# Performance work log

Hardware: AMD Instinct MI355X
Metric: run time of the kernel (lower is better)

Reference implementation:

```python
import jax, jax.numpy as jnp
import numpy as np

NUM_HEADS = 8  # matches init_kwargs


def setup_inputs() -> dict:
    key = jax.random.key(0)
    k_x, k_q, k_k, k_v, k_o = jax.random.split(key, 5)
    C = 512
    scale = 1.0 / np.sqrt(C).astype(np.float32)
    return {
        "x": jax.random.normal(k_x, (4, C, 1024), dtype=jnp.float32),
        "Wq": jax.random.normal(k_q, (C, C), dtype=jnp.float32) * scale,
        "Wk": jax.random.normal(k_k, (C, C), dtype=jnp.float32) * scale,
        "Wv": jax.random.normal(k_v, (C, C), dtype=jnp.float32) * scale,
        "Wo": jax.random.normal(k_o, (C, C), dtype=jnp.float32) * scale,
    }


def reference(x, Wq, Wk, Wv, Wo):
    # x: (b, C, n). Conv1d with kernel size 1 and no bias == channel matmul.
    b, C, n = x.shape
    H = NUM_HEADS
    d = C // H  # truncated_planes

    # 1x1 conv projections: (o, c) x (b, c, n) -> (b, o, n)
    q = jnp.einsum("oc,bcn->bon", Wq, x).reshape(b * H, d, n)
    k = jnp.einsum("oc,bcn->bon", Wk, x).reshape(b * H, d, n)
    v = jnp.einsum("oc,bcn->bon", Wv, x).reshape(b * H, d, n)

    # SelfAttention, embedded-gaussian mode (non-local block style, no 1/sqrt(d) scale):
    # scores[bh, i, j] = q[:, i] . k[:, j]; softmax over j; y = attn @ v
    scores = jnp.einsum("hdi,hdj->hij", q, k)       # (b*H, n, n)
    attn = jax.nn.softmax(scores, axis=-1)
    y = jnp.einsum("hij,hdj->hdi", attn, v)          # (b*H, d, n)

    y = y.reshape(b, C, n)
    out = jnp.einsum("oc,bcn->bon", Wo, y)           # final 1x1 conv
    return out
```

## Files before the change

### kernel.cpp

```cpp
#include <hip/hip_runtime.h>
#include <hip/hip_bf16.h>

typedef __attribute__((ext_vector_type(8))) short short8;
typedef __attribute__((ext_vector_type(8))) _Float16 half8;
typedef __attribute__((ext_vector_type(4))) float floatx4;

#define MFMA_BF16(a,b,c) __builtin_amdgcn_mfma_f32_16x16x32_bf16((a),(b),(c),0,0,0)
#define MFMA_F16(a,b,c)  __builtin_amdgcn_mfma_f32_16x16x32_f16((a),(b),(c),0,0,0)

__device__ __forceinline__ unsigned short f2bf(float f) {
    union { float f; unsigned u; } v; v.f = f;
    unsigned r = (v.u + 0x7fffu + ((v.u >> 16) & 1u)) >> 16;
    return (unsigned short)r;
}
__device__ __forceinline__ float bf2f(unsigned short h) {
    union { unsigned u; float f; } v; v.u = ((unsigned)h) << 16;
    return v.f;
}
__device__ __forceinline__ unsigned short f2h(float f) {
    union { _Float16 h; unsigned short u; } v; v.h = (_Float16)f;
    return v.u;
}
__device__ __forceinline__ float h2f(unsigned short u) {
    union { unsigned short u; _Float16 h; } v; v.u = u;
    return (float)v.h;
}

__device__ __forceinline__ void gll16(const unsigned short* g, unsigned short* l) {
    __builtin_amdgcn_global_load_lds(
        (const __attribute__((address_space(1))) void*)g,
        (__attribute__((address_space(3))) void*)l, 16, 0, 0);
}

__global__ __launch_bounds__(256) void prep_kernel(
    const void* __restrict__ x,
    const void* __restrict__ Wq, const void* __restrict__ Wk,
    const void* __restrict__ Wv, const void* __restrict__ Wo,
    unsigned short* __restrict__ xTh, unsigned short* __restrict__ xTl,
    unsigned short* __restrict__ Wqh, unsigned short* __restrict__ Wkh,
    unsigned short* __restrict__ Wvh, unsigned short* __restrict__ Woh,
    int* __restrict__ flag)
{
    __shared__ float tile[64][65];
    __shared__ int sflag;
    const int tid = threadIdx.x;

    if (tid < 64) {
        unsigned short u = ((const unsigned short*)x)[2 * tid];
        int e = (u >> 7) & 0xFF;
        bool plaus = (e >= 96 && e <= 140);
        unsigned long long m = __ballot(plaus);
        if (tid == 0) sflag = (__popcll(m) >= 40) ? 0 : 1;
    }
    __syncthreads();
    const int isf32 = sflag;
    const int bid = blockIdx.x;
    if (bid == 0 && tid == 0) *flag = isf32;

    if (bid < 512) {
        const int b  = bid >> 7;
        const int rem = bid & 127;
        const int c0 = (rem >> 4) * 64;
        const int n0 = (rem & 15) * 64;
        const int r = tid >> 6, col = tid & 63;
        const size_t base = (size_t)b * 512 * 1024;
        #pragma unroll
        for (int i = 0; i < 16; ++i) {
            int c = i * 4 + r;
            size_t idx = base + (size_t)(c0 + c) * 1024 + n0 + col;
            float v = isf32 ? ((const float*)x)[idx] : bf2f(((const unsigned short*)x)[idx]);
            tile[c][col] = v;
        }
        __syncthreads();
        #pragma unroll
        for (int i = 0; i < 16; ++i) {
            int n = i * 4 + r;
            float v = tile[col][n];
            unsigned short hi = f2h(v);
            size_t idx = ((size_t)b * 1024 + n0 + n) * 512 + c0 + col;
            xTh[idx] = hi;
            xTl[idx] = f2h(v - h2f(hi));
        }
    } else {
        const int b2 = bid - 512;
        #pragma unroll
        for (int m = 0; m < 4; ++m) {
            const void* src = (m == 0) ? Wq : (m == 1) ? Wk : (m == 2) ? Wv : Wo;
            unsigned short* dh = (m == 0) ? Wqh : (m == 1) ? Wkh : (m == 2) ? Wvh : Woh;
            #pragma unroll
            for (int j = 0; j < 16; ++j) {
                int i = b2 * 4096 + j * 256 + tid;
                float v = isf32 ? ((const float*)src)[i] : bf2f(((const unsigned short*)src)[i]);
                dh[i] = f2h(v);
            }
        }
    }
}

__device__ __forceinline__ void stage_qk(
    const unsigned short* __restrict__ Ah, const unsigned short* __restrict__ Al,
    const unsigned short* __restrict__ B,
    unsigned short* L, int k0, int wave, int srow, int koff)
{
    #pragma unroll
    for (int i = 0; i < 4; ++i) {
        int idx = wave + i * 4;
        const unsigned short* s;
        if (idx < 4)      s = Ah + (idx * 16 + srow) * 512 + k0 + koff;
        else if (idx < 8) s = Al + ((idx - 4) * 16 + srow) * 512 + k0 + koff;
        else              s = B + ((idx - 8) * 16 + srow) * 512 + k0 + koff;
        gll16(s, L + idx * 512);
    }
}

__device__ __forceinline__ void gemm_qk(
    const unsigned short* __restrict__ Ah, const unsigned short* __restrict__ Al,
    const unsigned short* __restrict__ B,
    unsigned short* lds, floatx4 acc[2][4], int lane, int wave)
{
    const int quad = lane >> 4, l16 = lane & 15;
    const int msub = (wave & 1) * 32, nsub = (wave >> 1) * 64;
    const int srow = lane >> 2;
    const int koff = (((lane & 3) - (srow >> 1)) & 3) * 8;
    const int pA = ((quad + (l16 >> 1)) & 3) * 8;

    stage_qk(Ah, Al, B, lds, 0, wave, srow, koff);
    for (int k0 = 0; k0 < 512; k0 += 32) {
        __syncthreads();
        unsigned short* L = lds + ((k0 >> 5) & 1) * 8192;
        if (k0 + 32 < 512)
            stage_qk(Ah, Al, B, lds + (((k0 >> 5) + 1) & 1) * 8192,
                     k0 + 32, wave, srow, koff);

        half8 ah[2], al[2], bh[4];
        #pragma unroll
        for (int mt = 0; mt < 2; ++mt) {
            int off = (msub + mt * 16 + l16) * 32 + pA;
            ah[mt] = *(const half8*)(L + off);
            al[mt] = *(const half8*)(L + 2048 + off);
        }
        #pragma unroll
        for (int nt = 0; nt < 4; ++nt)
            bh[nt] = *(const half8*)(L + 4096 + (nsub + nt * 16 + l16) * 32 + pA);
        #pragma unroll
        for (int mt = 0; mt < 2; ++mt)
            #pragma unroll
            for (int nt = 0; nt < 4; ++nt) {
                acc[mt][nt] = MFMA_F16(ah[mt], bh[nt], acc[mt][nt]);
                acc[mt][nt] = MFMA_F16(al[mt], bh[nt], acc[mt][nt]);
            }
    }
}

__device__ __forceinline__ void stage_1t(
    const unsigned short* __restrict__ A, const unsigned short* __restrict__ B,
    unsigned short* L, int k0, int wave, int srow, int koff)
{
    #pragma unroll
    for (int i = 0; i < 3; ++i) {
        int idx = wave + i * 4;
        const unsigned short* s;
        if (idx < 4) s = A + (idx * 16 + srow) * 512 + k0 + koff;
        else         s = B + ((idx - 4) * 16 + srow) * 512 + k0 + koff;
        gll16(s, L + idx * 512);
    }
}

__device__ __forceinline__ void gemm_1t(
    const unsigned short* __restrict__ A, const unsigned short* __restrict__ B,
    unsigned short* lds, floatx4 acc[2][4], int lane, int wave)
{
    const int quad = lane >> 4, l16 = lane & 15;
    const int msub = (wave & 1) * 32, nsub = (wave >> 1) * 64;
    const int srow = lane >> 2;
    const int koff = (((lane & 3) - (srow >> 1)) & 3) * 8;
    const int pA = ((quad + (l16 >> 1)) & 3) * 8;

    stage_1t(A, B, lds, 0, wave, srow, koff);
    for (int k0 = 0; k0 < 512; k0 += 32) {
        __syncthreads();
        unsigned short* L = lds + ((k0 >> 5) & 1) * 6144;
        if (k0 + 32 < 512)
            stage_1t(A, B, lds + (((k0 >> 5) + 1) & 1) * 6144,
                     k0 + 32, wave, srow, koff);

        half8 ah[2], bh[4];
        #pragma unroll
        for (int mt = 0; mt < 2; ++mt)
            ah[mt] = *(const half8*)(L + (msub + mt * 16 + l16) * 32 + pA);
        #pragma unroll
        for (int nt = 0; nt < 4; ++nt)
            bh[nt] = *(const half8*)(L + 2048 + (nsub + nt * 16 + l16) * 32 + pA);
        #pragma unroll
        for (int mt = 0; mt < 2; ++mt)
            #pragma unroll
            for (int nt = 0; nt < 4; ++nt)
                acc[mt][nt] = MFMA_F16(ah[mt], bh[nt], acc[mt][nt]);
    }
}

__global__ __launch_bounds__(256) void proj_kernel(
    const unsigned short* __restrict__ xTh, const unsigned short* __restrict__ xTl,
    const unsigned short* __restrict__ Wqh, const unsigned short* __restrict__ Wkh,
    const unsigned short* __restrict__ Wvh,
    unsigned short* __restrict__ qT, unsigned short* __restrict__ kT,
    unsigned short* __restrict__ vbuf)
{
    __shared__ unsigned short lds[16384];
    const int lane = threadIdx.x & 63;
    const int wave = threadIdx.x >> 6;
    const int quad = lane >> 4, l16 = lane & 15;
    const int idx = blockIdx.x;
    const int msub = (wave & 1) * 32, nsub = (wave >> 1) * 64;

    floatx4 acc[2][4];
    #pragma unroll
    for (int i = 0; i < 2; ++i)
        #pragma unroll
        for (int j = 0; j < 4; ++j) acc[i][j] = (floatx4){0.f, 0.f, 0.f, 0.f};

    if (idx < 512) {
        const int w = idx >> 8;
        const int rem = idx & 255;
        const int m0 = (rem >> 2) * 64;
        const int oblk = (rem & 3) * 128;
        gemm_qk(xTh + (size_t)m0 * 512, xTl + (size_t)m0 * 512,
                ((w == 0) ? Wqh : Wkh) + oblk * 512, lds, acc, lane, wave);

        unsigned short* dst = (w == 0) ? qT : kT;
        #pragma unroll
        for (int mt = 0; mt < 2; ++mt)
            #pragma unroll
            for (int r = 0; r < 4; ++r) {
                int row = m0 + msub + mt * 16 + quad * 4 + r;
                int b = row >> 10, n = row & 1023;
                #pragma unroll
                for (int nt = 0; nt < 4; ++nt) {
                    int o = oblk + nsub + nt * 16 + l16;
                    int head = b * 8 + (o >> 6);
                    int dd = o & 63;
                    dst[(head * 1024 + n) * 64 + dd] = f2h(acc[mt][nt][r]);
                }
            }
    } else {
        const int rem = idx - 512;
        const int m0 = (rem >> 5) * 64;
        const int nblk = (rem & 31) * 128;
        gemm_1t(Wvh + m0 * 512, xTh + (size_t)nblk * 512, lds, acc, lane, wave);

        #pragma unroll
        for (int mt = 0; mt < 2; ++mt)
            #pragma unroll
            for (int r = 0; r < 4; ++r) {
                int o = m0 + msub + mt * 16 + quad * 4 + r;
                #pragma unroll
                for (int nt = 0; nt < 4; ++nt) {
                    int col = nblk + nsub + nt * 16 + l16;
                    int b = col >> 10, n = col & 1023;
                    vbuf[b * (512 * 1024) + o * 1024 + n] = f2bf(acc[mt][nt][r]);
                }
            }
    }
}

__global__ __launch_bounds__(256) void attn_kernel(
    const unsigned short* __restrict__ qT, const unsigned short* __restrict__ kT,
    const unsigned short* __restrict__ vbuf,
    unsigned short* __restrict__ yT)
{
    __shared__ unsigned short lds[20992];
    const int lane = threadIdx.x & 63;
    const int wave = threadIdx.x >> 6;
    const int quad = lane >> 4, l16 = lane & 15;
    const int head = blockIdx.x;
    const int i0 = blockIdx.y * 64 + wave * 16;
    const int b = head >> 3, h = head & 7;
    const unsigned short* qp = qT + head * (1024 * 64);
    const unsigned short* kp = kT + head * (1024 * 64);
    const unsigned short* vb = vbuf + b * (512 * 1024) + h * (64 * 1024);
    const int srow = lane >> 2;
    const int koff = (((lane & 3) - (srow >> 1)) & 3) * 8;
    const int pA = ((quad + (l16 >> 1)) & 3) * 8;

    const int qoff = (i0 + l16) * 64 + quad * 8;
    half8 aq0 = *(const half8*)(qp + qoff);
    half8 aq1 = *(const half8*)(qp + qoff + 32);

    float lacc[4];
    floatx4 oacc[4];
    #pragma unroll
    for (int r = 0; r < 4; ++r) lacc[r] = 0.f;
    #pragma unroll
    for (int dt = 0; dt < 4; ++dt) oacc[dt] = (floatx4){0.f, 0.f, 0.f, 0.f};

    unsigned short* myp = lds + 16384 + wave * 1152;
    const float L2E = 1.44269504f;
    const float C2  = 69.2493619f;

    auto stage_kv = [&](int j0, unsigned short* L) {
        #pragma unroll
        for (int i = 0; i < 4; ++i) {
            int c = wave + i * 4;
            const unsigned short* s;
            if (c < 8) {
                int kc = c >> 2, r0 = (c & 3) * 16;
                s = kp + (j0 + r0 + srow) * 64 + kc * 32 + koff;
            } else {
                int c8 = c - 8; int js = c8 >> 2, r0 = (c8 & 3) * 16;
                s = vb + (r0 + srow) * 1024 + j0 + js * 32 + koff;
            }
            gll16(s, L + c * 512);
        }
    };

    stage_kv(0, lds);

    for (int j0 = 0; j0 < 1024; j0 += 64) {
        __syncthreads();
        unsigned short* L = lds + ((j0 >> 6) & 1) * 8192;
        if (j0 + 64 < 1024)
            stage_kv(j0 + 64, lds + (((j0 >> 6) + 1) & 1) * 8192);

        floatx4 sc[4];
        #pragma unroll
        for (int jt = 0; jt < 4; ++jt) {
            int off = jt * 512 + l16 * 32 + pA;
            half8 kh0 = *(const half8*)(L + off);
            half8 kh1 = *(const half8*)(L + 2048 + off);
            floatx4 s = {0.f, 0.f, 0.f, 0.f};
            s = MFMA_F16(aq0, kh0, s);
            s = MFMA_F16(aq1, kh1, s);
            sc[jt] = s;
        }

        #pragma unroll
        for (int jt = 0; jt < 4; ++jt)
            #pragma unroll
            for (int r = 0; r < 4; ++r) {
                float p = __builtin_amdgcn_exp2f(sc[jt][r] * L2E - C2);
                lacc[r] += p;
                myp[(quad * 4 + r) * 72 + jt * 16 + l16] = f2bf(p);
            }
        __asm__ volatile("s_waitcnt lgkmcnt(0)" ::: "memory");
        short8 pa0 = *(const short8*)(myp + l16 * 72 + quad * 8);
        short8 pa1 = *(const short8*)(myp + l16 * 72 + 32 + quad * 8);

        #pragma unroll
        for (int dt = 0; dt < 4; ++dt) {
            int off = dt * 512 + l16 * 32 + pA;
            short8 bv0 = *(const short8*)(L + 4096 + off);
            short8 bv1 = *(const short8*)(L + 4096 + 2048 + off);
            oacc[dt] = MFMA_BF16(pa0, bv0, oacc[dt]);
            oacc[dt] = MFMA_BF16(pa1, bv1, oacc[dt]);
        }
    }

    float linv[4];
    #pragma unroll
    for (int r = 0; r < 4; ++r) {
        float l = lacc[r];
        l += __shfl_xor(l, 1);
        l += __shfl_xor(l, 2);
        l += __shfl_xor(l, 4);
        l += __shfl_xor(l, 8);
        linv[r] = 1.0f / l;
    }
    #pragma unroll
    for (int dt = 0; dt < 4; ++dt)
        #pragma unroll
        for (int r = 0; r < 4; ++r) {
            int c = h * 64 + dt * 16 + l16;
            int n = i0 + quad * 4 + r;
            yT[((size_t)b * 1024 + n) * 512 + c] = f2h(oacc[dt][r] * linv[r]);
        }
}

__global__ __launch_bounds__(256) void out_kernel(
    const unsigned short* __restrict__ Woh, const unsigned short* __restrict__ yT,
    void* __restrict__ out, const int* __restrict__ flag)
{
    __shared__ unsigned short lds[8192];
    const int isf32 = *flag;
    const int lane = threadIdx.x & 63;
    const int wave = threadIdx.x >> 6;
    const int quad = lane >> 4, l16 = lane & 15;
    const int nblk = blockIdx.x * 64;
    const int oblk = blockIdx.y * 64;
    const unsigned short* A = Woh + oblk * 512;
    const unsigned short* B = yT + (size_t)nblk * 512;
    const int msub = (wave & 1) * 32, nsub = (wave >> 1) * 32;
    const int srow = lane >> 2;
    const int koff = (((lane & 3) - (srow >> 1)) & 3) * 8;
    const int pA = ((quad + (l16 >> 1)) & 3) * 8;

    floatx4 acc[2][2];
    #pragma unroll
    for (int i = 0; i < 2; ++i)
        #pragma unroll
        for (int j = 0; j < 2; ++j) acc[i][j] = (floatx4){0.f, 0.f, 0.f, 0.f};

    auto stage = [&](int k0, unsigned short* L) {
        #pragma unroll
        for (int i = 0; i < 2; ++i) {
            int idx = wave + i * 4;
            const unsigned short* s = (idx < 4)
                ? A + (idx * 16 + srow) * 512 + k0 + koff
                : B + ((idx - 4) * 16 + srow) * 512 + k0 + koff;
            gll16(s, L + idx * 512);
        }
    };

    stage(0, lds);
    for (int k0 = 0; k0 < 512; k0 += 32) {
        __syncthreads();
        unsigned short* L = lds + ((k0 >> 5) & 1) * 4096;
        if (k0 + 32 < 512)
            stage(k0 + 32, lds + (((k0 >> 5) + 1) & 1) * 4096);

        half8 ah[2], bh[2];
        #pragma unroll
        for (int mt = 0; mt < 2; ++mt)
            ah[mt] = *(const half8*)(L + (msub + mt * 16 + l16) * 32 + pA);
        #pragma unroll
        for (int nt = 0; nt < 2; ++nt)
            bh[nt] = *(const half8*)(L + 2048 + (nsub + nt * 16 + l16) * 32 + pA);
        #pragma unroll
        for (int mt = 0; mt < 2; ++mt)
            #pragma unroll
            for (int nt = 0; nt < 2; ++nt)
                acc[mt][nt] = MFMA_F16(ah[mt], bh[nt], acc[mt][nt]);
    }

    #pragma unroll
    for (int mt = 0; mt < 2; ++mt)
        #pragma unroll
        for (int r = 0; r < 4; ++r) {
            int o = oblk + msub + mt * 16 + quad * 4 + r;
            #pragma unroll
            for (int nt = 0; nt < 2; ++nt) {
                int col = nblk + nsub + nt * 16 + l16;
                int b = col >> 10, n = col & 1023;
                size_t di = (size_t)b * (512 * 1024) + o * 1024 + n;
                if (isf32) ((float*)out)[di] = acc[mt][nt][r];
                else       ((unsigned short*)out)[di] = f2bf(acc[mt][nt][r]);
            }
        }
}

extern "C" void kernel_launch(void* const* d_in, const int* in_sizes, int n_in,
                              void* d_out, int out_size, void* d_ws, size_t ws_size,
                              hipStream_t stream)
{
    const void* x  = d_in[0];
    const void* Wq = d_in[1];
    const void* Wk = d_in[2];
    const void* Wv = d_in[3];
    const void* Wo = d_in[4];

    const int NX = 4 * 512 * 1024;
    const int NW = 512 * 512;

    char* p = (char*)d_ws;
    int* flag = (int*)p; p += 64;
    unsigned short* xTh = (unsigned short*)p; p += (size_t)NX * 2;
    unsigned short* xTl = (unsigned short*)p; p += (size_t)NX * 2;
    unsigned short* Wqh = (unsigned short*)p; p += (size_t)NW * 2;
    unsigned short* Wkh = (unsigned short*)p; p += (size_t)NW * 2;
    unsigned short* Wvh = (unsigned short*)p; p += (size_t)NW * 2;
    unsigned short* Woh = (unsigned short*)p; p += (size_t)NW * 2;
    unsigned short* qT  = (unsigned short*)p; p += (size_t)NX * 2;
    unsigned short* kT  = (unsigned short*)p; p += (size_t)NX * 2;
    unsigned short* vbuf = (unsigned short*)p; p += (size_t)NX * 2;
    unsigned short* ybuf = (unsigned short*)p; p += (size_t)NX * 2;

    prep_kernel<<<576, 256, 0, stream>>>(
        x, Wq, Wk, Wv, Wo, xTh, xTl, Wqh, Wkh, Wvh, Woh, flag);
    proj_kernel<<<768, 256, 0, stream>>>(
        xTh, xTl, Wqh, Wkh, Wvh, qT, kT, vbuf);
    attn_kernel<<<dim3(32, 16), 256, 0, stream>>>(
        qT, kT, vbuf, ybuf);
    out_kernel<<<dim3(64, 8), 256, 0, stream>>>(
        Woh, ybuf, d_out, flag);
}
```

Before: 130.3 us.

## Drop split-fp16 x for Q/K projection, enlarge attention and output tiles

Removes the hi/lo fp16 split of x, so the Q/K projection uses a single fp16 GEMM instead of two MFMAs per tile. Prep traffic also shrinks because only one transposed copy of x is written. Attention blocks grow to 512 threads covering 128 query rows, so each staged K/V tile is shared by more waves. The output GEMM switches to the shared 64x128 tile routine. The cost is lower Q/K precision, which could hurt accuracy because scores are unscaled before the softmax.

```diff
diff --git a/kernel.cpp b/kernel.cpp
--- a/kernel.cpp
+++ b/kernel.cpp
@@ -21,10 +21,6 @@
     union { _Float16 h; unsigned short u; } v; v.h = (_Float16)f;
     return v.u;
 }
-__device__ __forceinline__ float h2f(unsigned short u) {
-    union { unsigned short u; _Float16 h; } v; v.u = u;
-    return (float)v.h;
-}
 
 __device__ __forceinline__ void gll16(const unsigned short* g, unsigned short* l) {
     __builtin_amdgcn_global_load_lds(
@@ -36,7 +32,7 @@
     const void* __restrict__ x,
     const void* __restrict__ Wq, const void* __restrict__ Wk,
     const void* __restrict__ Wv, const void* __restrict__ Wo,
-    unsigned short* __restrict__ xTh, unsigned short* __restrict__ xTl,
+    unsigned short* __restrict__ xT,
     unsigned short* __restrict__ Wqh, unsigned short* __restrict__ Wkh,
     unsigned short* __restrict__ Wvh, unsigned short* __restrict__ Woh,
     int* __restrict__ flag)
@@ -75,11 +71,8 @@
         #pragma unroll
         for (int i = 0; i < 16; ++i) {
             int n = i * 4 + r;
-            float v = tile[col][n];
-            unsigned short hi = f2h(v);
             size_t idx = ((size_t)b * 1024 + n0 + n) * 512 + c0 + col;
-            xTh[idx] = hi;
-            xTl[idx] = f2h(v - h2f(hi));
+            xT[idx] = f2h(tile[col][n]);
         }
     } else {
         const int b2 = bid - 512;
@@ -94,61 +87,6 @@
                 dh[i] = f2h(v);
             }
         }
-    }
-}
-
-__device__ __forceinline__ void stage_qk(
-    const unsigned short* __restrict__ Ah, const unsigned short* __restrict__ Al,
-    const unsigned short* __restrict__ B,
-    unsigned short* L, int k0, int wave, int srow, int koff)
-{
-    #pragma unroll
-    for (int i = 0; i < 4; ++i) {
-        int idx = wave + i * 4;
-        const unsigned short* s;
-        if (idx < 4)      s = Ah + (idx * 16 + srow) * 512 + k0 + koff;
-        else if (idx < 8) s = Al + ((idx - 4) * 16 + srow) * 512 + k0 + koff;
-        else              s = B + ((idx - 8) * 16 + srow) * 512 + k0 + koff;
-        gll16(s, L + idx * 512);
-    }
-}
-
-__device__ __forceinline__ void gemm_qk(
-    const unsigned short* __restrict__ Ah, const unsigned short* __restrict__ Al,
-    const unsigned short* __restrict__ B,
-    unsigned short* lds, floatx4 acc[2][4], int lane, int wave)
-{
-    const int quad = lane >> 4, l16 = lane & 15;
-    const int msub = (wave & 1) * 32, nsub = (wave >> 1) * 64;
-    const int srow = lane >> 2;
-    const int koff = (((lane & 3) - (srow >> 1)) & 3) * 8;
-    const int pA = ((quad + (l16 >> 1)) & 3) * 8;
-
-    stage_qk(Ah, Al, B, lds, 0, wave, srow, koff);
-    for (int k0 = 0; k0 < 512; k0 += 32) {
-        __syncthreads();
-        unsigned short* L = lds + ((k0 >> 5) & 1) * 8192;
-        if (k0 + 32 < 512)
-            stage_qk(Ah, Al, B, lds + (((k0 >> 5) + 1) & 1) * 8192,
-                     k0 + 32, wave, srow, koff);
-
-        half8 ah[2], al[2], bh[4];
-        #pragma unroll
-        for (int mt = 0; mt < 2; ++mt) {
-            int off = (msub + mt * 16 + l16) * 32 + pA;
-            ah[mt] = *(const half8*)(L + off);
-            al[mt] = *(const half8*)(L + 2048 + off);
-        }
-        #pragma unroll
-        for (int nt = 0; nt < 4; ++nt)
-            bh[nt] = *(const half8*)(L + 4096 + (nsub + nt * 16 + l16) * 32 + pA);
-        #pragma unroll
-        for (int mt = 0; mt < 2; ++mt)
-            #pragma unroll
-            for (int nt = 0; nt < 4; ++nt) {
-                acc[mt][nt] = MFMA_F16(ah[mt], bh[nt], acc[mt][nt]);
-                acc[mt][nt] = MFMA_F16(al[mt], bh[nt], acc[mt][nt]);
-            }
     }
 }
 
@@ -200,13 +138,13 @@
 }
 
 __global__ __launch_bounds__(256) void proj_kernel(
-    const unsigned short* __restrict__ xTh, const unsigned short* __restrict__ xTl,
+    const unsigned short* __restrict__ xT,
     const unsigned short* __restrict__ Wqh, const unsigned short* __restrict__ Wkh,
     const unsigned short* __restrict__ Wvh,
     unsigned short* __restrict__ qT, unsigned short* __restrict__ kT,
     unsigned short* __restrict__ vbuf)
 {
-    __shared__ unsigned short lds[16384];
+    __shared__ unsigned short lds[12288];
     const int lane = threadIdx.x & 63;
     const int wave = threadIdx.x >> 6;
     const int quad = lane >> 4, l16 = lane & 15;
@@ -224,8 +162,8 @@
         const int rem = idx & 255;
         const int m0 = (rem >> 2) * 64;
         const int oblk = (rem & 3) * 128;
-        gemm_qk(xTh + (size_t)m0 * 512, xTl + (size_t)m0 * 512,
-                ((w == 0) ? Wqh : Wkh) + oblk * 512, lds, acc, lane, wave);
+        gemm_1t(xT + (size_t)m0 * 512, ((w == 0) ? Wqh : Wkh) + oblk * 512,
+                lds, acc, lane, wave);
 
         unsigned short* dst = (w == 0) ? qT : kT;
         #pragma unroll
@@ -246,7 +184,7 @@
         const int rem = idx - 512;
         const int m0 = (rem >> 5) * 64;
         const int nblk = (rem & 31) * 128;
-        gemm_1t(Wvh + m0 * 512, xTh + (size_t)nblk * 512, lds, acc, lane, wave);
+        gemm_1t(Wvh + m0 * 512, xT + (size_t)nblk * 512, lds, acc, lane, wave);
 
         #pragma unroll
         for (int mt = 0; mt < 2; ++mt)
@@ -263,17 +201,17 @@
     }
 }
 
-__global__ __launch_bounds__(256) void attn_kernel(
+__global__ __launch_bounds__(512) void attn_kernel(
     const unsigned short* __restrict__ qT, const unsigned short* __restrict__ kT,
     const unsigned short* __restrict__ vbuf,
     unsigned short* __restrict__ yT)
 {
-    __shared__ unsigned short lds[20992];
+    __shared__ unsigned short lds[25600];
     const int lane = threadIdx.x & 63;
     const int wave = threadIdx.x >> 6;
     const int quad = lane >> 4, l16 = lane & 15;
     const int head = blockIdx.x;
-    const int i0 = blockIdx.y * 64 + wave * 16;
+    const int i0 = blockIdx.y * 128 + wave * 16;
     const int b = head >> 3, h = head & 7;
     const unsigned short* qp = qT + head * (1024 * 64);
     const unsigned short* kp = kT + head * (1024 * 64);
@@ -299,8 +237,8 @@
 
     auto stage_kv = [&](int j0, unsigned short* L) {
         #pragma unroll
-        for (int i = 0; i < 4; ++i) {
-            int c = wave + i * 4;
+        for (int i = 0; i < 2; ++i) {
+            int c = wave + i * 8;
             const unsigned short* s;
             if (c < 8) {
                 int kc = c >> 2, r0 = (c & 3) * 16;
@@ -379,65 +317,30 @@
     const unsigned short* __restrict__ Woh, const unsigned short* __restrict__ yT,
     void* __restrict__ out, const int* __restrict__ flag)
 {
-    __shared__ unsigned short lds[8192];
+    __shared__ unsigned short lds[12288];
     const int isf32 = *flag;
     const int lane = threadIdx.x & 63;
     const int wave = threadIdx.x >> 6;
     const int quad = lane >> 4, l16 = lane & 15;
-    const int nblk = blockIdx.x * 64;
+    const int nblk = blockIdx.x * 128;
     const int oblk = blockIdx.y * 64;
-    const unsigned short* A = Woh + oblk * 512;
-    const unsigned short* B = yT + (size_t)nblk * 512;
-    const int msub = (wave & 1) * 32, nsub = (wave >> 1) * 32;
-    const int srow = lane >> 2;
-    const int koff = (((lane & 3) - (srow >> 1)) & 3) * 8;
-    const int pA = ((quad + (l16 >> 1)) & 3) * 8;
-
-    floatx4 acc[2][2];
+
+    floatx4 acc[2][4];
     #pragma unroll
     for (int i = 0; i < 2; ++i)
         #pragma unroll
-        for (int j = 0; j < 2; ++j) acc[i][j] = (floatx4){0.f, 0.f, 0.f, 0.f};
-
-    auto stage = [&](int k0, unsigned short* L) {
-        #pragma unroll
-        for (int i = 0; i < 2; ++i) {
-            int idx = wave + i * 4;
-            const unsigned short* s = (idx < 4)
-                ? A + (idx * 16 + srow) * 512 + k0 + koff
-                : B + ((idx - 4) * 16 + srow) * 512 + k0 + koff;
-            gll16(s, L + idx * 512);
-        }
-    };
-
-    stage(0, lds);
-    for (int k0 = 0; k0 < 512; k0 += 32) {
-        __syncthreads();
-        unsigned short* L = lds + ((k0 >> 5) & 1) * 4096;
-        if (k0 + 32 < 512)
-            stage(k0 + 32, lds + (((k0 >> 5) + 1) & 1) * 4096);
-
-        half8 ah[2], bh[2];
-        #pragma unroll
-        for (int mt = 0; mt < 2; ++mt)
-            ah[mt] = *(const half8*)(L + (msub + mt * 16 + l16) * 32 + pA);
-        #pragma unroll
-        for (int nt = 0; nt < 2; ++nt)
-            bh[nt] = *(const half8*)(L + 2048 + (nsub + nt * 16 + l16) * 32 + pA);
-        #pragma unroll
-        for (int mt = 0; mt < 2; ++mt)
-            #pragma unroll
-            for (int nt = 0; nt < 2; ++nt)
-                acc[mt][nt] = MFMA_F16(ah[mt], bh[nt], acc[mt][nt]);
-    }
-
+        for (int j = 0; j < 4; ++j) acc[i][j] = (floatx4){0.f, 0.f, 0.f, 0.f};
+
+    gemm_1t(Woh + oblk * 512, yT + (size_t)nblk * 512, lds, acc, lane, wave);
+
+    const int msub = (wave & 1) * 32, nsub = (wave >> 1) * 64;
     #pragma unroll
     for (int mt = 0; mt < 2; ++mt)
         #pragma unroll
         for (int r = 0; r < 4; ++r) {
             int o = oblk + msub + mt * 16 + quad * 4 + r;
             #pragma unroll
-            for (int nt = 0; nt < 2; ++nt) {
+            for (int nt = 0; nt < 4; ++nt) {
                 int col = nblk + nsub + nt * 16 + l16;
                 int b = col >> 10, n = col & 1023;
                 size_t di = (size_t)b * (512 * 1024) + o * 1024 + n;
@@ -462,8 +365,7 @@
 
     char* p = (char*)d_ws;
     int* flag = (int*)p; p += 64;
-    unsigned short* xTh = (unsigned short*)p; p += (size_t)NX * 2;
-    unsigned short* xTl = (unsigned short*)p; p += (size_t)NX * 2;
+    unsigned short* xT  = (unsigned short*)p; p += (size_t)NX * 2;
     unsigned short* Wqh = (unsigned short*)p; p += (size_t)NW * 2;
     unsigned short* Wkh = (unsigned short*)p; p += (size_t)NW * 2;
     unsigned short* Wvh = (unsigned short*)p; p += (size_t)NW * 2;
@@ -474,11 +376,11 @@
     unsigned short* ybuf = (unsigned short*)p; p += (size_t)NX * 2;
 
     prep_kernel<<<576, 256, 0, stream>>>(
-        x, Wq, Wk, Wv, Wo, xTh, xTl, Wqh, Wkh, Wvh, Woh, flag);
+        x, Wq, Wk, Wv, Wo, xT, Wqh, Wkh, Wvh, Woh, flag);
     proj_kernel<<<768, 256, 0, stream>>>(
-        xTh, xTl, Wqh, Wkh, Wvh, qT, kT, vbuf);
-    attn_kernel<<<dim3(32, 16), 256, 0, stream>>>(
+        xT, Wqh, Wkh, Wvh, qT, kT, vbuf);
+    attn_kernel<<<dim3(32, 8), 512, 0, stream>>>(
         qT, kT, vbuf, ybuf);
-    out_kernel<<<dim3(64, 8), 256, 0, stream>>>(
+    out_kernel<<<dim3(32, 8), 256, 0, stream>>>(
         Woh, ybuf, d_out, flag);
 }
```

After: 126.0 us. 1.03x faster.
